# Kernel optimization log

Hardware: AMD Instinct MI355X
Metric: run time of the kernel (lower is better)

Reference implementation:

```python
import jax, jax.numpy as jnp
import numpy as np

N, E = 50000, 800000
H, C, K = 8, 16, 4
LAMBD = 1.0
DECAY = [float(np.log(LAMBD / (k + 1) + (1 + 1e-06))) for k in range(K + 1)]


def setup_inputs() -> dict:
    key = jax.random.key(0)
    ks = jax.random.split(key, 10)
    s = 0.05  # keep activations stable over K hops
    return {
        "x": jax.random.normal(ks[0], (N, 256), jnp.float32),
        "edge_index": jax.random.randint(ks[1], (2, E), 0, N, jnp.int64),
        "W0": jax.random.normal(ks[2], (256, 128), jnp.float32) * s,
        "b0": jnp.zeros((128,), jnp.float32),
        "W1": jax.random.normal(ks[3], (128, 128), jnp.float32) * s,
        "b1": jnp.zeros((128,), jnp.float32),
        "Wout": jax.random.normal(ks[4], (128, 40), jnp.float32) * s,
        "bout": jnp.zeros((40,), jnp.float32),
        "hop_att0": jax.random.normal(ks[5], (H, C), jnp.float32) * s,
        "hop_atts": jax.random.normal(ks[6], (K, H, 2 * C), jnp.float32) * s,
        "atts": jax.random.normal(ks[7], (K, H, C), jnp.float32) * s,
        "hop_biases": jnp.ones((K + 1, H), jnp.float32),
    }


def _aero_forward(x, edge_index, W0, b0, W1, b1, Wout, bout,
                  hop_att0, hop_atts, atts, hop_biases):
    n = x.shape[0]
    # add self loops (cached_edge_index is None in the torch module)
    loops = jnp.arange(n, dtype=edge_index.dtype)
    row = jnp.concatenate([edge_index[0], loops])  # source j
    col = jnp.concatenate([edge_index[1], loops])  # target i

    # hid_feat_init (dropout p=0 -> identity); num_layers=2
    h = x @ W0 + b0
    h = jax.nn.elu(h) @ W1 + b1
    h = h.reshape(n, H, C)

    # k = 0 hop attention
    g = jnp.einsum('hc,nhc->nh', hop_att0, jax.nn.elu(h)) + hop_biases[0]
    z = h * g[..., None]
    z_scale = z * DECAY[0]

    for k in range(1, K + 1):
        # edge attention: gather, elementwise, degree-normalize
        zi = z_scale[col]          # [E', H, C] target
        zj = z_scale[row]          # [E', H, C] source
        a = jnp.einsum('hc,ehc->eh', atts[k - 1], jax.nn.elu(zi + zj))
        a = jax.nn.softplus(a) + 1e-06                       # [E', H]
        deg = jax.ops.segment_sum(a, col, num_segments=n)    # [N, H]
        dinv = jnp.where(deg > 0, deg ** -0.5, 0.0)
        a = dinv[row] * a * dinv[col]
        # propagate: scatter-add weighted source features onto targets
        h = jax.ops.segment_sum(a[..., None] * h[row], col, num_segments=n)
        # hop attention on concat(h, z_scale)
        hz = jax.nn.elu(jnp.concatenate([h, z_scale], axis=-1))  # [N, H, 2C]
        g = jnp.einsum('hc,nhc->nh', hop_atts[k - 1], hz) + hop_biases[k]
        z = z + h * g[..., None]
        z_scale = z * DECAY[k]

    # node classifier
    z = jax.nn.elu(z.reshape(n, H * C))
    return z @ Wout + bout


def reference(x, edge_index, W0, b0, W1, b1, Wout, bout,
              hop_att0, hop_atts, atts, hop_biases):
    return _aero_forward(x, edge_index, W0, b0, W1, b1, Wout, bout,
                         hop_att0, hop_atts, atts, hop_biases)
```

## Files before the change

kernel.cpp:

```cpp
#include <hip/hip_runtime.h>
#include <hip/hip_fp16.h>
#include <math.h>

#define NH 8
#define NC 16
#define HC 128
#define CAPB 12288

typedef __attribute__((ext_vector_type(8))) _Float16 half8;
typedef __attribute__((ext_vector_type(4))) float f32x4;

__device__ __forceinline__ float eluf(float x) { return x > 0.f ? x : __expf(x) - 1.f; }
__device__ __forceinline__ float splusf(float x) { return fmaxf(x, 0.f) + __logf(1.f + __expf(-fabsf(x))); }

#if __has_builtin(__builtin_amdgcn_exp2f)
#define EXP2F(x) __builtin_amdgcn_exp2f(x)
#else
#define EXP2F(x) exp2f(x)
#endif

template <typename T>
__device__ __forceinline__ T ntload(const T* p) { return __builtin_nontemporal_load(p); }
template <typename T>
__device__ __forceinline__ void ntstore(T* p, T v) { __builtin_nontemporal_store(v, p); }

__global__ __launch_bounds__(256)
void csr1_kernel(const int* __restrict__ ei, uint2* __restrict__ pairs,
                 int* __restrict__ gCnt, int E, int E2) {
    __shared__ int h1[256];
    __shared__ int bbase[256];
    __shared__ int cur[256];
    const int t = threadIdx.x;
    const int e0 = blockIdx.x * 4096;
    int rows[16], cols[16];
#pragma unroll
    for (int i = 0; i < 16; ++i) {
        int e = e0 + i * 256 + t;
        int r = 0, c = -1;
        if (e < E) { r = ei[e]; c = ei[E + e]; }
        else if (e < E2) { r = e - E; c = e - E; }
        rows[i] = r; cols[i] = c;
    }
    h1[t] = 0; cur[t] = 0;
    __syncthreads();
#pragma unroll
    for (int i = 0; i < 16; ++i)
        if (cols[i] >= 0) atomicAdd(&h1[cols[i] >> 8], 1);
    __syncthreads();
    if (h1[t] > 0) bbase[t] = atomicAdd(&gCnt[t], h1[t]);
    __syncthreads();
#pragma unroll
    for (int i = 0; i < 16; ++i) {
        if (cols[i] >= 0) {
            int b = cols[i] >> 8;
            int r = atomicAdd(&cur[b], 1);
            int pos = bbase[b] + r;
            if (pos < CAPB)
                pairs[(size_t)b * CAPB + pos] =
                    make_uint2((unsigned)rows[i], (unsigned)cols[i]);
        }
    }
}

__global__ void scanbkt_kernel(const int* __restrict__ gCnt, int* __restrict__ bktPtr,
                               int NBKT) {
    __shared__ int tmp[256];
    int t = threadIdx.x;
    int v = (t < NBKT) ? gCnt[t] : 0;
    tmp[t] = v;
    __syncthreads();
    for (int off = 1; off < 256; off <<= 1) {
        int add = (t >= off) ? tmp[t - off] : 0;
        __syncthreads();
        tmp[t] += add;
        __syncthreads();
    }
    if (t < NBKT) bktPtr[t] = tmp[t] - v;
}

__global__ __launch_bounds__(256)
void csr2_kernel(const uint2* __restrict__ pairs, const int* __restrict__ gCnt,
                 const int* __restrict__ bktPtr, int* __restrict__ ptr,
                 int* __restrict__ src, int N, int NBKT, int E2) {
    __shared__ int hist[256];
    __shared__ int scanb[256];
    __shared__ int cur[256];
    __shared__ int stage[CAPB];
    const int b = blockIdx.x;
    const int t = threadIdx.x;
    const int c0 = b << 8;
    int cnt = gCnt[b]; if (cnt > CAPB) cnt = CAPB;
    const int base = bktPtr[b];
    hist[t] = 0; cur[t] = 0;
    __syncthreads();
    const uint2* bp = pairs + (size_t)b * CAPB;
    for (int idx = t; idx < cnt; idx += 256) {
        int c = (int)bp[idx].y - c0;
        atomicAdd(&hist[c], 1);
    }
    __syncthreads();
    int v = hist[t];
    scanb[t] = v;
    __syncthreads();
    for (int off = 1; off < 256; off <<= 1) {
        int add = (t >= off) ? scanb[t - off] : 0;
        __syncthreads();
        scanb[t] += add;
        __syncthreads();
    }
    int excl = scanb[t] - v;
    int ncols = N - c0; if (ncols > 256) ncols = 256;
    if (t < ncols) ptr[c0 + t] = base + excl;
    if (b == NBKT - 1 && t == 0) ptr[N] = E2;
    __syncthreads();
    scanb[t] = excl;
    __syncthreads();
    for (int idx = t; idx < cnt; idx += 256) {
        uint2 u = bp[idx];
        int c = (int)u.y - c0;
        int r = atomicAdd(&cur[c], 1);
        stage[scanb[c] + r] = (int)u.x;
    }
    __syncthreads();
    for (int idx = t; idx < cnt; idx += 256)
        ntstore(&src[base + idx], stage[idx]);
}

__global__ void wswz_kernel(const float* __restrict__ W, _Float16* __restrict__ Wf, int NKS) {
    int t = blockIdx.x * 256 + threadIdx.x;
    if (t >= 8 * NKS * 64) return;
    int lane = t & 63;
    int ks = (t >> 6) % NKS;
    int cg = (t >> 6) / NKS;
    int n = cg * 16 + (lane & 15);
    int k0 = ks * 32 + (lane >> 4) * 8;
    half8 v;
#pragma unroll
    for (int j = 0; j < 8; ++j) v[j] = (_Float16)W[(size_t)(k0 + j) * 128 + n];
    *(half8*)(Wf + (size_t)t * 8) = v;
}

template<int K, bool A16, bool HOP0>
__global__ __launch_bounds__(256)
void mfma_gemm(const float* __restrict__ A32, const _Float16* __restrict__ A16p,
               const _Float16* __restrict__ Wf, const float* __restrict__ bias,
               int M, _Float16* __restrict__ h1_out,
               float* __restrict__ z_out, _Float16* __restrict__ h16_out,
               _Float16* __restrict__ z16_out,
               const float* __restrict__ att0, const float* __restrict__ hb0) {
    constexpr int NKS = K / 32;
    __shared__ float sL[64 * 132];
    const int tid = threadIdx.x;
    const int w = tid >> 6;
    const int lane = tid & 63;
    const int l15 = lane & 15;
    const int lg = lane >> 4;
    const int m0 = blockIdx.x * 64;

    f32x4 acc[4][2];
#pragma unroll
    for (int a = 0; a < 4; ++a)
#pragma unroll
        for (int b = 0; b < 2; ++b)
            acc[a][b] = f32x4{0.f, 0.f, 0.f, 0.f};

#pragma unroll
    for (int ks = 0; ks < NKS; ++ks) {
        const int kb = ks * 32 + lg * 8;
        half8 af[4];
        if (A16) {
#pragma unroll
            for (int mf = 0; mf < 4; ++mf) {
                int row = m0 + mf * 16 + l15;
                af[mf] = *(const half8*)(A16p + ((size_t)row << 7) + kb);
            }
        } else {
#pragma unroll
            for (int mf = 0; mf < 4; ++mf) {
                int row = m0 + mf * 16 + l15;
                float4 a0 = make_float4(0.f, 0.f, 0.f, 0.f), a1 = a0;
                if (row < M) {
                    const float* ap = A32 + (size_t)row * K + kb;
                    a0 = *(const float4*)ap;
                    a1 = *(const float4*)(ap + 4);
                }
                half8 h;
                h[0] = (_Float16)a0.x; h[1] = (_Float16)a0.y;
                h[2] = (_Float16)a0.z; h[3] = (_Float16)a0.w;
                h[4] = (_Float16)a1.x; h[5] = (_Float16)a1.y;
                h[6] = (_Float16)a1.z; h[7] = (_Float16)a1.w;
                af[mf] = h;
            }
        }
        half8 bf[2];
#pragma unroll
        for (int cf = 0; cf < 2; ++cf) {
            int cg = w * 2 + cf;
            bf[cf] = *(const half8*)(Wf + (size_t)((cg * NKS + ks) * 64 + lane) * 8);
        }
#pragma unroll
        for (int mf = 0; mf < 4; ++mf)
#pragma unroll
            for (int cf = 0; cf < 2; ++cf)
                acc[mf][cf] = __builtin_amdgcn_mfma_f32_16x16x32_f16(af[mf], bf[cf],
                                                                     acc[mf][cf], 0, 0, 0);
    }

#pragma unroll
    for (int mf = 0; mf < 4; ++mf)
#pragma unroll
        for (int cf = 0; cf < 2; ++cf) {
            int col = w * 32 + cf * 16 + l15;
#pragma unroll
            for (int r = 0; r < 4; ++r)
                sL[(mf * 16 + lg * 4 + r) * 132 + col] = acc[mf][cf][r];
        }
    __syncthreads();

    const int rr = lane;
    const int q = w;
    const int row = m0 + rr;
    float v[32];
#pragma unroll
    for (int t = 0; t < 8; ++t)
        *(float4*)&v[t * 4] = *(const float4*)&sL[rr * 132 + q * 32 + t * 4];
#pragma unroll
    for (int t = 0; t < 8; ++t) {
        float4 bv = *(const float4*)&bias[q * 32 + t * 4];
        v[t * 4 + 0] += bv.x; v[t * 4 + 1] += bv.y;
        v[t * 4 + 2] += bv.z; v[t * 4 + 3] += bv.w;
    }

    if (!HOP0) {
        if (row < M) {
            half8 o[4];
#pragma unroll
            for (int c = 0; c < 32; ++c) o[c >> 3][c & 7] = (_Float16)eluf(v[c]);
            _Float16* hp = h1_out + ((size_t)row << 7) + q * 32;
#pragma unroll
            for (int t = 0; t < 4; ++t) *(half8*)(hp + t * 8) = o[t];
        }
    } else {
        float g[2];
#pragma unroll
        for (int hh = 0; hh < 2; ++hh) {
            int head = q * 2 + hh;
            float p = 0.f;
#pragma unroll
            for (int c = 0; c < 16; ++c)
                p = fmaf(att0[head * 16 + c], eluf(v[hh * 16 + c]), p);
            g[hh] = p + hb0[head];
        }
        if (row < M) {
            float zz[32];
#pragma unroll
            for (int c = 0; c < 32; ++c) zz[c] = v[c] * g[c >> 4];
            half8 ho[4], zo[4];
#pragma unroll
            for (int c = 0; c < 32; ++c) {
                ho[c >> 3][c & 7] = (_Float16)v[c];
                zo[c >> 3][c & 7] = (_Float16)zz[c];
            }
            _Float16* hp  = h16_out + ((size_t)row << 7) + q * 32;
            _Float16* zhp = z16_out + ((size_t)row << 7) + q * 32;
            float*    zp  = z_out   + ((size_t)row << 7) + q * 32;
#pragma unroll
            for (int t = 0; t < 4; ++t) {
                *(half8*)(hp + t * 8) = ho[t];
                *(half8*)(zhp + t * 8) = zo[t];
            }
#pragma unroll
            for (int t = 0; t < 8; ++t)
                *(float4*)(zp + t * 4) = make_float4(zz[t * 4 + 0], zz[t * 4 + 1],
                                                     zz[t * 4 + 2], zz[t * 4 + 3]);
        }
    }
}

__global__ __launch_bounds__(256)
void passA_kernel(const _Float16* __restrict__ z16, const int* __restrict__ ptr,
                  const int* __restrict__ src, const float* __restrict__ att,
                  float decay, _Float16* __restrict__ a_e, float* __restrict__ dinv, int n) {
    int wid = (int)((blockIdx.x * 256u + threadIdx.x) >> 6);
    if (wid >= n) return;
    const int lane = threadIdx.x & 63;
    const int g  = lane >> 4;
    const int q  = lane & 15;
    const int hd = q >> 1;
    const unsigned i = (unsigned)wid;
    const float dl2 = decay * 1.44269504089f;

    float ziL[8];
    {
        const half8 zi = *(const half8*)(z16 + ((size_t)i << 7) + (q << 3));
#pragma unroll
        for (int c = 0; c < 8; ++c) ziL[c] = (float)zi[c] * dl2;
    }
    float av[8];
    *(float4*)&av[0] = *(const float4*)(att + (q << 3));
    *(float4*)&av[4] = *(const float4*)(att + (q << 3) + 4);
    float sav = ((av[0] + av[1]) + (av[2] + av[3]))
              + ((av[4] + av[5]) + (av[6] + av[7]));
    sav += __shfl_xor(sav, 1);

    const int s0 = ptr[wid], s1 = ptr[wid + 1];
    float dacc = 0.f;

#define PA_BODY(f, sv) do {                                                  \
        float pm = 0.f, pe = 0.f;                                            \
        _Pragma("unroll")                                                    \
        for (int c = 0; c < 8; ++c) {                                        \
            float y = fmaf((float)(f)[c], dl2, ziL[c]);                      \
            float e2 = EXP2F(fminf(y, 0.f));                                 \
            pm = fmaf(av[c], fmaxf(y, 0.f), pm);                             \
            pe = fmaf(av[c], e2, pe);                                        \
        }                                                                    \
        float pc = fmaf(pm, 0.69314718056f, pe);                             \
        pc += __shfl_xor(pc, 1);                                             \
        if ((q & 1) == 0) {                                                  \
            float aval = splusf(pc - sav) + 1e-6f;                           \
            ntstore(&a_e[((size_t)(sv) << 3) + hd], (_Float16)aval);         \
            dacc += aval;                                                    \
        }                                                                    \
    } while (0)

    const int nfull = (s1 - s0) & ~7;
    const int send = s0 + nfull;
    for (int s = s0 + g; s < send; s += 8) {
        unsigned ja = (unsigned)ntload(&src[s]);
        unsigned jb = (unsigned)ntload(&src[s + 4]);
        const half8 fa = *(const half8*)(z16 + ((size_t)ja << 7) + (q << 3));
        const half8 fb = *(const half8*)(z16 + ((size_t)jb << 7) + (q << 3));
        PA_BODY(fa, s);
        PA_BODY(fb, s + 4);
    }
    {
        int sA = send + g;
        if (sA < s1) {
            unsigned ja = (unsigned)src[sA];
            const half8 fa = *(const half8*)(z16 + ((size_t)ja << 7) + (q << 3));
            PA_BODY(fa, sA);
        }
        int sB = send + 4 + g;
        if (sB < s1) {
            unsigned jb = (unsigned)src[sB];
            const half8 fb = *(const half8*)(z16 + ((size_t)jb << 7) + (q << 3));
            PA_BODY(fb, sB);
        }
    }
#undef PA_BODY

    dacc += __shfl_xor(dacc, 16);
    dacc += __shfl_xor(dacc, 32);
    if ((lane & 0x31) == 0) {
        dinv[((size_t)i << 3) + hd] = (dacc > 0.f) ? (1.f / sqrtf(dacc)) : 0.f;
    }
}

__global__ __launch_bounds__(256)
void passB_kernel(const _Float16* __restrict__ h_in, float* __restrict__ z,
                  _Float16* __restrict__ z16,
                  const int* __restrict__ ptr, const int* __restrict__ src,
                  const _Float16* __restrict__ a_e, const float* __restrict__ dinv,
                  const float* __restrict__ hatt, const float* __restrict__ hb,
                  float decay, _Float16* __restrict__ h_out, int n, int store_h) {
    int wid = (int)((blockIdx.x * 256u + threadIdx.x) >> 6);
    if (wid >= n) return;
    const int lane = threadIdx.x & 63;
    const int g  = lane >> 4;
    const int q  = lane & 15;
    const int hd = q >> 1;
    const unsigned i = (unsigned)wid;

    const float di = dinv[((size_t)i << 3) + hd];
    const int s0 = ptr[wid], s1 = ptr[wid + 1];
    float acc[8];
#pragma unroll
    for (int c = 0; c < 8; ++c) acc[c] = 0.f;

    const int nfull = (s1 - s0) & ~7;
    const int send = s0 + nfull;
    for (int s = s0 + g; s < send; s += 8) {
        unsigned ja = (unsigned)ntload(&src[s]);
        unsigned jb = (unsigned)ntload(&src[s + 4]);
        const _Float16 aA = ntload(&a_e[((size_t)s << 3) + hd]);
        const _Float16 aB = ntload(&a_e[((size_t)(s + 4) << 3) + hd]);
        const float dA = dinv[((size_t)ja << 3) + hd];
        const float dB = dinv[((size_t)jb << 3) + hd];
        const half8 fa = *(const half8*)(h_in + ((size_t)ja << 7) + (q << 3));
        const half8 fb = *(const half8*)(h_in + ((size_t)jb << 7) + (q << 3));
        const float wa = (float)aA * dA;
        const float wb = (float)aB * dB;
#pragma unroll
        for (int c = 0; c < 8; ++c) acc[c] = fmaf((float)fa[c], wa, acc[c]);
#pragma unroll
        for (int c = 0; c < 8; ++c) acc[c] = fmaf((float)fb[c], wb, acc[c]);
    }
    {
        int sA = send + g;
        if (sA < s1) {
            unsigned j = (unsigned)src[sA];
            const float w = (float)a_e[((size_t)sA << 3) + hd] * dinv[((size_t)j << 3) + hd];
            const half8 f = *(const half8*)(h_in + ((size_t)j << 7) + (q << 3));
#pragma unroll
            for (int c = 0; c < 8; ++c) acc[c] = fmaf((float)f[c], w, acc[c]);
        }
        int sB = send + 4 + g;
        if (sB < s1) {
            unsigned j = (unsigned)src[sB];
            const float w = (float)a_e[((size_t)sB << 3) + hd] * dinv[((size_t)j << 3) + hd];
            const half8 f = *(const half8*)(h_in + ((size_t)j << 7) + (q << 3));
#pragma unroll
            for (int c = 0; c < 8; ++c) acc[c] = fmaf((float)f[c], w, acc[c]);
        }
    }
    float* zrow = z + ((size_t)i << 7) + (q << 3);
    const f32x4 zva = ntload((const f32x4*)zrow);
    const f32x4 zvb = ntload((const f32x4*)(zrow + 4));
#pragma unroll
    for (int c = 0; c < 8; ++c) {
        acc[c] += __shfl_xor(acc[c], 16);
        acc[c] += __shfl_xor(acc[c], 32);
    }

    if (g == 0) {
        float hn[8];
#pragma unroll
        for (int c = 0; c < 8; ++c) hn[c] = di * acc[c];
        float zv[8] = {zva.x, zva.y, zva.z, zva.w, zvb.x, zvb.y, zvb.z, zvb.w};

        const float* hA = hatt + hd * 32 + (q & 1) * 8;
        float p = 0.f;
#pragma unroll
        for (int c = 0; c < 8; ++c) p = fmaf(hA[c], eluf(hn[c]), p);
#pragma unroll
        for (int c = 0; c < 8; ++c) p = fmaf(hA[16 + c], eluf(zv[c] * decay), p);
        p += __shfl_xor(p, 1);
        const float gv = p + hb[hd];

        float zn[8];
#pragma unroll
        for (int c = 0; c < 8; ++c) zn[c] = fmaf(hn[c], gv, zv[c]);
        ntstore((f32x4*)zrow, f32x4{zn[0], zn[1], zn[2], zn[3]});
        ntstore((f32x4*)(zrow + 4), f32x4{zn[4], zn[5], zn[6], zn[7]});
        if (store_h) {
            half8 ho, zo;
#pragma unroll
            for (int c = 0; c < 8; ++c) { ho[c] = (_Float16)hn[c]; zo[c] = (_Float16)zn[c]; }
            ntstore((half8*)(h_out + ((size_t)i << 7) + (q << 3)), ho);
            ntstore((half8*)(z16   + ((size_t)i << 7) + (q << 3)), zo);
        }
    }
}

__global__ __launch_bounds__(256)
void gout_kernel(const float* __restrict__ z, const float* __restrict__ W,
                 const float* __restrict__ bias, float* __restrict__ out, int M) {
    __shared__ float zs[128 * 65];
    __shared__ float ws[128 * 40];
    const int tid = threadIdx.x;
    const int r0 = blockIdx.x * 64;
    for (int idx = tid; idx < 128 * 40; idx += 256) ws[idx] = W[idx];
    const int r = tid >> 2;
    const int q = tid & 3;
    {
        int grow = r0 + r;
#pragma unroll
        for (int t = 0; t < 8; ++t) {
            int k = q * 4 + t * 16;
            f32x4 v = f32x4{0.f, 0.f, 0.f, 0.f};
            if (grow < M) v = ntload((const f32x4*)(z + (size_t)grow * HC + k));
            zs[(k + 0) * 65 + r] = eluf(v.x);
            zs[(k + 1) * 65 + r] = eluf(v.y);
            zs[(k + 2) * 65 + r] = eluf(v.z);
            zs[(k + 3) * 65 + r] = eluf(v.w);
        }
    }
    __syncthreads();
    float acc[10];
#pragma unroll
    for (int j = 0; j < 10; ++j) acc[j] = bias[q * 10 + j];
    for (int k = 0; k < 128; ++k) {
        float zk = zs[k * 65 + r];
#pragma unroll
        for (int j = 0; j < 10; ++j)
            acc[j] = fmaf(zk, ws[k * 40 + q * 10 + j], acc[j]);
    }
    int grow = r0 + r;
    if (grow < M) {
        float* op = out + (size_t)grow * 40 + q * 10;
#pragma unroll
        for (int j = 0; j < 10; ++j) op[j] = acc[j];
    }
}

extern "C" void kernel_launch(void* const* d_in, const int* in_sizes, int n_in,
                              void* d_out, int out_size, void* d_ws, size_t ws_size,
                              hipStream_t stream) {
    (void)n_in; (void)out_size; (void)ws_size;
    const float* x    = (const float*)d_in[0];
    const int*   ei   = (const int*)d_in[1];
    const float* W0   = (const float*)d_in[2];
    const float* b0   = (const float*)d_in[3];
    const float* W1   = (const float*)d_in[4];
    const float* b1   = (const float*)d_in[5];
    const float* Wout = (const float*)d_in[6];
    const float* bout = (const float*)d_in[7];
    const float* att0 = (const float*)d_in[8];
    const float* hatts= (const float*)d_in[9];
    const float* atts = (const float*)d_in[10];
    const float* hb   = (const float*)d_in[11];
    float* out = (float*)d_out;

    const int N  = in_sizes[0] / 256;
    const int E  = in_sizes[1] / 2;
    const int E2 = E + N;
    const int NBKT = (N + 255) >> 8;
    const size_t Npad = ((size_t)N + 63) & ~(size_t)63;

    char* p = (char*)d_ws;
    auto carve = [&](size_t bytes) -> char* {
        char* r = p;
        p += (bytes + 255) & ~(size_t)255;
        return r;
    };
    _Float16* h1     = (_Float16*)carve(Npad * HC * 2);
    _Float16* hbufA  = (_Float16*)carve((size_t)N * HC * 2);
    _Float16* hbufB  = (_Float16*)carve((size_t)N * HC * 2);
    float*    zbuf   = (float*)carve((size_t)N * HC * 4);
    _Float16* z16buf = (_Float16*)carve((size_t)N * HC * 2);
    _Float16* a_e    = (_Float16*)carve((size_t)E2 * NH * 2);
    float*    dinvb  = (float*)carve((size_t)N * NH * 4);
    _Float16* Wf0    = (_Float16*)carve((size_t)8 * 8 * 64 * 8 * 2);
    _Float16* Wf1    = (_Float16*)carve((size_t)8 * 4 * 64 * 8 * 2);
    int* csr_ptr   = (int*)carve((size_t)(N + 1) * 4);
    int* csr_src   = (int*)carve((size_t)E2 * 4);
    int* gCnt      = (int*)carve(256 * 4);
    int* bktPtr    = (int*)carve(257 * 4);
    uint2* pairs = (uint2*)zbuf;

    float decay[5];
    for (int k = 0; k <= 4; ++k) decay[k] = (float)log(1.0 / (k + 1) + 1.0 + 1e-6);

    hipMemsetAsync(gCnt, 0, 256 * 4, stream);
    int b1n = (E2 + 4095) / 4096;
    csr1_kernel<<<b1n, 256, 0, stream>>>(ei, pairs, gCnt, E, E2);
    scanbkt_kernel<<<1, 256, 0, stream>>>(gCnt, bktPtr, NBKT);
    csr2_kernel<<<NBKT, 256, 0, stream>>>(pairs, gCnt, bktPtr, csr_ptr, csr_src,
                                          N, NBKT, E2);

    wswz_kernel<<<16, 256, 0, stream>>>(W0, Wf0, 8);
    wswz_kernel<<<8, 256, 0, stream>>>(W1, Wf1, 4);

    int gb = (N + 63) / 64;
    mfma_gemm<256, false, false><<<gb, 256, 0, stream>>>(
        x, nullptr, Wf0, b0, N, h1, nullptr, nullptr, nullptr, nullptr, nullptr);
    mfma_gemm<128, true, true><<<gb, 256, 0, stream>>>(
        nullptr, h1, Wf1, b1, N, nullptr, zbuf, hbufA, z16buf, att0, hb);

    _Float16* hin  = hbufA;
    _Float16* hout = hbufB;
    int wb = (N + 3) / 4;
    for (int k = 1; k <= 4; ++k) {
        passA_kernel<<<wb, 256, 0, stream>>>(z16buf, csr_ptr, csr_src,
                                             atts + (size_t)(k - 1) * NH * NC,
                                             decay[k - 1], a_e, dinvb, N);
        passB_kernel<<<wb, 256, 0, stream>>>(hin, zbuf, z16buf, csr_ptr, csr_src,
                                             a_e, dinvb,
                                             hatts + (size_t)(k - 1) * NH * 32,
                                             hb + (size_t)k * NH, decay[k - 1], hout, N,
                                             (k < 4) ? 1 : 0);
        _Float16* t = hin; hin = hout; hout = t;
    }

    gout_kernel<<<(N + 63) / 64, 256, 0, stream>>>(zbuf, Wout, bout, out, N);
}
```

Before: 638.6 us.

## Sort nodes by in-degree and remap wave-to-node assignment in edge passes

Adds a counting-sort pass that buckets nodes by in-degree (capped at 63) into a permutation array. passA and passB then map each wavefront to perm[wid] instead of wid, so waves within a block handle nodes of similar degree. This is meant to cut load imbalance and tail divergence among co-resident waves. It costs three extra small kernels plus a memset per call, and it scatters the node access order, which can hurt locality on z/h row writes and on ptr reads.

```diff
diff --git a/kernel.cpp b/kernel.cpp
--- a/kernel.cpp
+++ b/kernel.cpp
@@ -6,6 +6,7 @@
 #define NC 16
 #define HC 128
 #define CAPB 12288
+#define DBIN 64
 
 typedef __attribute__((ext_vector_type(8))) _Float16 half8;
 typedef __attribute__((ext_vector_type(4))) float f32x4;
@@ -124,6 +125,60 @@
     __syncthreads();
     for (int idx = t; idx < cnt; idx += 256)
         ntstore(&src[base + idx], stage[idx]);
+}
+
+__global__ __launch_bounds__(256)
+void deg1_kernel(const int* __restrict__ ptr, int* __restrict__ gdh, int N) {
+    __shared__ int h[DBIN];
+    int t = threadIdx.x, i = blockIdx.x * 256 + t;
+    if (t < DBIN) h[t] = 0;
+    __syncthreads();
+    if (i < N) {
+        int d = ptr[i + 1] - ptr[i];
+        if (d > DBIN - 1) d = DBIN - 1;
+        atomicAdd(&h[d], 1);
+    }
+    __syncthreads();
+    if (t < DBIN && h[t] > 0) atomicAdd(&gdh[t], h[t]);
+}
+
+__global__ void degscan_kernel(const int* __restrict__ gdh, int* __restrict__ gdcur) {
+    __shared__ int tmp[DBIN];
+    int t = threadIdx.x;
+    int v = gdh[t];
+    tmp[t] = v;
+    __syncthreads();
+    for (int off = 1; off < DBIN; off <<= 1) {
+        int a = (t >= off) ? tmp[t - off] : 0;
+        __syncthreads();
+        tmp[t] += a;
+        __syncthreads();
+    }
+    gdcur[t] = tmp[t] - v;
+}
+
+__global__ __launch_bounds__(256)
+void deg2_kernel(const int* __restrict__ ptr, int* __restrict__ gdcur,
+                 int* __restrict__ perm, int N) {
+    __shared__ int h[DBIN];
+    __shared__ int base[DBIN];
+    __shared__ int cur[DBIN];
+    int t = threadIdx.x, i = blockIdx.x * 256 + t;
+    if (t < DBIN) { h[t] = 0; cur[t] = 0; }
+    __syncthreads();
+    int d = -1;
+    if (i < N) {
+        d = ptr[i + 1] - ptr[i];
+        if (d > DBIN - 1) d = DBIN - 1;
+        atomicAdd(&h[d], 1);
+    }
+    __syncthreads();
+    if (t < DBIN && h[t] > 0) base[t] = atomicAdd(&gdcur[t], h[t]);
+    __syncthreads();
+    if (i < N) {
+        int r = atomicAdd(&cur[d], 1);
+        perm[base[d] + r] = i;
+    }
 }
 
 __global__ void wswz_kernel(const float* __restrict__ W, _Float16* __restrict__ Wf, int NKS) {
@@ -279,10 +334,12 @@
 
 __global__ __launch_bounds__(256)
 void passA_kernel(const _Float16* __restrict__ z16, const int* __restrict__ ptr,
-                  const int* __restrict__ src, const float* __restrict__ att,
+                  const int* __restrict__ src, const int* __restrict__ perm,
+                  const float* __restrict__ att,
                   float decay, _Float16* __restrict__ a_e, float* __restrict__ dinv, int n) {
-    int wid = (int)((blockIdx.x * 256u + threadIdx.x) >> 6);
-    if (wid >= n) return;
+    int widRaw = (int)((blockIdx.x * 256u + threadIdx.x) >> 6);
+    if (widRaw >= n) return;
+    const int wid = perm[widRaw];
     const int lane = threadIdx.x & 63;
     const int g  = lane >> 4;
     const int q  = lane & 15;
@@ -361,11 +418,13 @@
 void passB_kernel(const _Float16* __restrict__ h_in, float* __restrict__ z,
                   _Float16* __restrict__ z16,
                   const int* __restrict__ ptr, const int* __restrict__ src,
+                  const int* __restrict__ perm,
                   const _Float16* __restrict__ a_e, const float* __restrict__ dinv,
                   const float* __restrict__ hatt, const float* __restrict__ hb,
                   float decay, _Float16* __restrict__ h_out, int n, int store_h) {
-    int wid = (int)((blockIdx.x * 256u + threadIdx.x) >> 6);
-    if (wid >= n) return;
+    int widRaw = (int)((blockIdx.x * 256u + threadIdx.x) >> 6);
+    if (widRaw >= n) return;
+    const int wid = perm[widRaw];
     const int lane = threadIdx.x & 63;
     const int g  = lane >> 4;
     const int q  = lane & 15;
@@ -537,17 +596,26 @@
     int* csr_src   = (int*)carve((size_t)E2 * 4);
     int* gCnt      = (int*)carve(256 * 4);
     int* bktPtr    = (int*)carve(257 * 4);
+    int* gdh       = (int*)carve(DBIN * 4);
+    int* gdcur     = (int*)carve(DBIN * 4);
+    int* permb     = (int*)carve((size_t)N * 4);
     uint2* pairs = (uint2*)zbuf;
 
     float decay[5];
     for (int k = 0; k <= 4; ++k) decay[k] = (float)log(1.0 / (k + 1) + 1.0 + 1e-6);
 
     hipMemsetAsync(gCnt, 0, 256 * 4, stream);
+    hipMemsetAsync(gdh, 0, DBIN * 4, stream);
     int b1n = (E2 + 4095) / 4096;
+    int nb = (N + 255) / 256;
     csr1_kernel<<<b1n, 256, 0, stream>>>(ei, pairs, gCnt, E, E2);
     scanbkt_kernel<<<1, 256, 0, stream>>>(gCnt, bktPtr, NBKT);
     csr2_kernel<<<NBKT, 256, 0, stream>>>(pairs, gCnt, bktPtr, csr_ptr, csr_src,
                                           N, NBKT, E2);
+
+    deg1_kernel<<<nb, 256, 0, stream>>>(csr_ptr, gdh, N);
+    degscan_kernel<<<1, DBIN, 0, stream>>>(gdh, gdcur);
+    deg2_kernel<<<nb, 256, 0, stream>>>(csr_ptr, gdcur, permb, N);
 
     wswz_kernel<<<16, 256, 0, stream>>>(W0, Wf0, 8);
     wswz_kernel<<<8, 256, 0, stream>>>(W1, Wf1, 4);
@@ -562,10 +630,10 @@
     _Float16* hout = hbufB;
     int wb = (N + 3) / 4;
     for (int k = 1; k <= 4; ++k) {
-        passA_kernel<<<wb, 256, 0, stream>>>(z16buf, csr_ptr, csr_src,
+        passA_kernel<<<wb, 256, 0, stream>>>(z16buf, csr_ptr, csr_src, permb,
                                              atts + (size_t)(k - 1) * NH * NC,
                                              decay[k - 1], a_e, dinvb, N);
-        passB_kernel<<<wb, 256, 0, stream>>>(hin, zbuf, z16buf, csr_ptr, csr_src,
+        passB_kernel<<<wb, 256, 0, stream>>>(hin, zbuf, z16buf, csr_ptr, csr_src, permb,
                                              a_e, dinvb,
                                              hatts + (size_t)(k - 1) * NH * 32,
                                              hb + (size_t)k * NH, decay[k - 1], hout, N,
```

Result: slower. 668.9 us (+4.8%).

## Fuse output classifier into final propagation pass and pack CSR pairs into 32 bits

Applied to the files above, without the earlier changes.

The final hop's passB kernel now computes the updated z, applies ELU and multiplies by Wout (staged in shared memory) directly, writing logits. This removes the separate gout kernel and the last write and reread of the fp32 z buffer. Separately, the CSR bucket pairs are packed into one 32-bit word (source index shifted left by 8, low 8 bits of the target), which halves the scratch traffic in csr1 and csr2. Every lane in the fused path does the output GEMV, and every block loads 20KB of weights into LDS on the last hop, which adds LDS pressure. The packing only works while source indices fit in 24 bits.

```diff
diff --git a/kernel.cpp b/kernel.cpp
--- a/kernel.cpp
+++ b/kernel.cpp
@@ -25,7 +25,7 @@
 __device__ __forceinline__ void ntstore(T* p, T v) { __builtin_nontemporal_store(v, p); }
 
 __global__ __launch_bounds__(256)
-void csr1_kernel(const int* __restrict__ ei, uint2* __restrict__ pairs,
+void csr1_kernel(const int* __restrict__ ei, unsigned* __restrict__ pairs,
                  int* __restrict__ gCnt, int E, int E2) {
     __shared__ int h1[256];
     __shared__ int bbase[256];
@@ -57,7 +57,7 @@
             int pos = bbase[b] + r;
             if (pos < CAPB)
                 pairs[(size_t)b * CAPB + pos] =
-                    make_uint2((unsigned)rows[i], (unsigned)cols[i]);
+                    ((unsigned)rows[i] << 8) | ((unsigned)cols[i] & 255u);
         }
     }
 }
@@ -79,7 +79,7 @@
 }
 
 __global__ __launch_bounds__(256)
-void csr2_kernel(const uint2* __restrict__ pairs, const int* __restrict__ gCnt,
+void csr2_kernel(const unsigned* __restrict__ pairs, const int* __restrict__ gCnt,
                  const int* __restrict__ bktPtr, int* __restrict__ ptr,
                  int* __restrict__ src, int N, int NBKT, int E2) {
     __shared__ int hist[256];
@@ -93,9 +93,9 @@
     const int base = bktPtr[b];
     hist[t] = 0; cur[t] = 0;
     __syncthreads();
-    const uint2* bp = pairs + (size_t)b * CAPB;
+    const unsigned* bp = pairs + (size_t)b * CAPB;
     for (int idx = t; idx < cnt; idx += 256) {
-        int c = (int)bp[idx].y - c0;
+        int c = (int)(bp[idx] & 255u);
         atomicAdd(&hist[c], 1);
     }
     __syncthreads();
@@ -116,10 +116,10 @@
     scanb[t] = excl;
     __syncthreads();
     for (int idx = t; idx < cnt; idx += 256) {
-        uint2 u = bp[idx];
-        int c = (int)u.y - c0;
+        unsigned u = bp[idx];
+        int c = (int)(u & 255u);
         int r = atomicAdd(&cur[c], 1);
-        stage[scanb[c] + r] = (int)u.x;
+        stage[scanb[c] + r] = (int)(u >> 8);
     }
     __syncthreads();
     for (int idx = t; idx < cnt; idx += 256)
@@ -363,10 +363,19 @@
                   const int* __restrict__ ptr, const int* __restrict__ src,
                   const _Float16* __restrict__ a_e, const float* __restrict__ dinv,
                   const float* __restrict__ hatt, const float* __restrict__ hb,
-                  float decay, _Float16* __restrict__ h_out, int n, int store_h) {
-    int wid = (int)((blockIdx.x * 256u + threadIdx.x) >> 6);
-    if (wid >= n) return;
-    const int lane = threadIdx.x & 63;
+                  float decay, _Float16* __restrict__ h_out, int n,
+                  const float* __restrict__ Wout, const float* __restrict__ bout,
+                  float* __restrict__ outp, int fuse_out) {
+    __shared__ float ws[HC * 40];
+    const int tid = threadIdx.x;
+    int wid = (int)((blockIdx.x * 256u + tid) >> 6);
+    const bool active = wid < n;
+    if (fuse_out) {
+        for (int idx = tid; idx < HC * 40; idx += 256) ws[idx] = Wout[idx];
+        __syncthreads();
+    }
+    if (!active) return;
+    const int lane = tid & 63;
     const int g  = lane >> 4;
     const int q  = lane & 15;
     const int hd = q >> 1;
@@ -423,11 +432,12 @@
         acc[c] += __shfl_xor(acc[c], 32);
     }
 
-    if (g == 0) {
-        float hn[8];
+    if (fuse_out) {
+        float hn[8], zv[8];
 #pragma unroll
         for (int c = 0; c < 8; ++c) hn[c] = di * acc[c];
-        float zv[8] = {zva.x, zva.y, zva.z, zva.w, zvb.x, zvb.y, zvb.z, zvb.w};
+        zv[0] = zva.x; zv[1] = zva.y; zv[2] = zva.z; zv[3] = zva.w;
+        zv[4] = zvb.x; zv[5] = zvb.y; zv[6] = zvb.z; zv[7] = zvb.w;
 
         const float* hA = hatt + hd * 32 + (q & 1) * 8;
         float p = 0.f;
@@ -438,59 +448,56 @@
         p += __shfl_xor(p, 1);
         const float gv = p + hb[hd];
 
+        float ez[8];
+#pragma unroll
+        for (int c = 0; c < 8; ++c) ez[c] = eluf(fmaf(hn[c], gv, zv[c]));
+
+        float po[10];
+#pragma unroll
+        for (int j = 0; j < 10; ++j) po[j] = 0.f;
+#pragma unroll
+        for (int c = 0; c < 8; ++c) {
+            const float* wr = &ws[(q * 8 + c) * 40 + g * 10];
+#pragma unroll
+            for (int j = 0; j < 10; ++j) po[j] = fmaf(ez[c], wr[j], po[j]);
+        }
+#pragma unroll
+        for (int j = 0; j < 10; ++j) {
+            po[j] += __shfl_xor(po[j], 1);
+            po[j] += __shfl_xor(po[j], 2);
+            po[j] += __shfl_xor(po[j], 4);
+            po[j] += __shfl_xor(po[j], 8);
+        }
+        if (q == 0) {
+            float* op = outp + (size_t)wid * 40 + g * 10;
+#pragma unroll
+            for (int j = 0; j < 10; ++j) op[j] = po[j] + bout[g * 10 + j];
+        }
+    } else if (g == 0) {
+        float hn[8];
+#pragma unroll
+        for (int c = 0; c < 8; ++c) hn[c] = di * acc[c];
+        float zv[8] = {zva.x, zva.y, zva.z, zva.w, zvb.x, zvb.y, zvb.z, zvb.w};
+
+        const float* hA = hatt + hd * 32 + (q & 1) * 8;
+        float p = 0.f;
+#pragma unroll
+        for (int c = 0; c < 8; ++c) p = fmaf(hA[c], eluf(hn[c]), p);
+#pragma unroll
+        for (int c = 0; c < 8; ++c) p = fmaf(hA[16 + c], eluf(zv[c] * decay), p);
+        p += __shfl_xor(p, 1);
+        const float gv = p + hb[hd];
+
         float zn[8];
 #pragma unroll
         for (int c = 0; c < 8; ++c) zn[c] = fmaf(hn[c], gv, zv[c]);
         ntstore((f32x4*)zrow, f32x4{zn[0], zn[1], zn[2], zn[3]});
         ntstore((f32x4*)(zrow + 4), f32x4{zn[4], zn[5], zn[6], zn[7]});
-        if (store_h) {
-            half8 ho, zo;
-#pragma unroll
-            for (int c = 0; c < 8; ++c) { ho[c] = (_Float16)hn[c]; zo[c] = (_Float16)zn[c]; }
-            ntstore((half8*)(h_out + ((size_t)i << 7) + (q << 3)), ho);
-            ntstore((half8*)(z16   + ((size_t)i << 7) + (q << 3)), zo);
-        }
-    }
-}
-
-__global__ __launch_bounds__(256)
-void gout_kernel(const float* __restrict__ z, const float* __restrict__ W,
-                 const float* __restrict__ bias, float* __restrict__ out, int M) {
-    __shared__ float zs[128 * 65];
-    __shared__ float ws[128 * 40];
-    const int tid = threadIdx.x;
-    const int r0 = blockIdx.x * 64;
-    for (int idx = tid; idx < 128 * 40; idx += 256) ws[idx] = W[idx];
-    const int r = tid >> 2;
-    const int q = tid & 3;
-    {
-        int grow = r0 + r;
-#pragma unroll
-        for (int t = 0; t < 8; ++t) {
-            int k = q * 4 + t * 16;
-            f32x4 v = f32x4{0.f, 0.f, 0.f, 0.f};
-            if (grow < M) v = ntload((const f32x4*)(z + (size_t)grow * HC + k));
-            zs[(k + 0) * 65 + r] = eluf(v.x);
-            zs[(k + 1) * 65 + r] = eluf(v.y);
-            zs[(k + 2) * 65 + r] = eluf(v.z);
-            zs[(k + 3) * 65 + r] = eluf(v.w);
-        }
-    }
-    __syncthreads();
-    float acc[10];
-#pragma unroll
-    for (int j = 0; j < 10; ++j) acc[j] = bias[q * 10 + j];
-    for (int k = 0; k < 128; ++k) {
-        float zk = zs[k * 65 + r];
-#pragma unroll
-        for (int j = 0; j < 10; ++j)
-            acc[j] = fmaf(zk, ws[k * 40 + q * 10 + j], acc[j]);
-    }
-    int grow = r0 + r;
-    if (grow < M) {
-        float* op = out + (size_t)grow * 40 + q * 10;
-#pragma unroll
-        for (int j = 0; j < 10; ++j) op[j] = acc[j];
+        half8 ho, zo;
+#pragma unroll
+        for (int c = 0; c < 8; ++c) { ho[c] = (_Float16)hn[c]; zo[c] = (_Float16)zn[c]; }
+        ntstore((half8*)(h_out + ((size_t)i << 7) + (q << 3)), ho);
+        ntstore((half8*)(z16   + ((size_t)i << 7) + (q << 3)), zo);
     }
 }
 
@@ -537,7 +544,7 @@
     int* csr_src   = (int*)carve((size_t)E2 * 4);
     int* gCnt      = (int*)carve(256 * 4);
     int* bktPtr    = (int*)carve(257 * 4);
-    uint2* pairs = (uint2*)zbuf;
+    unsigned* pairs = (unsigned*)zbuf;
 
     float decay[5];
     for (int k = 0; k <= 4; ++k) decay[k] = (float)log(1.0 / (k + 1) + 1.0 + 1e-6);
@@ -569,9 +576,7 @@
                                              a_e, dinvb,
                                              hatts + (size_t)(k - 1) * NH * 32,
                                              hb + (size_t)k * NH, decay[k - 1], hout, N,
-                                             (k < 4) ? 1 : 0);
+                                             Wout, bout, out, (k == 4) ? 1 : 0);
         _Float16* t = hin; hin = hout; hout = t;
     }
-
-    gout_kernel<<<(N + 63) / 64, 256, 0, stream>>>(zbuf, Wout, bout, out, N);
-}
+}
```

After: 811.1 us. +27.0%, slower.
